# Kernel tuning notes

Hardware: AMD Instinct MI355X
Metric: run time of the kernel (lower is better)

Reference implementation:

```python
import jax, jax.numpy as jnp
import numpy as np

B, D, F, K = 16384, 768, 8192, 32

def setup_inputs() -> dict:
    key = jax.random.key(0)
    k0, k1, k2 = jax.random.split(key, 3)
    x = jax.random.normal(k0, (B, D), dtype=jnp.float32)
    # encoder weight ~ orthogonal-ish scale; exact init scheme doesn't affect the math being tested
    W_enc = jax.random.normal(k1, (F, D), dtype=jnp.float32) / np.sqrt(D)
    b_enc = jnp.zeros((F,), dtype=jnp.float32)
    W_dec = jax.random.normal(k2, (D, F), dtype=jnp.float32)
    # torch init normalizes decoder.weight rows (dim=1)
    W_dec = W_dec / jnp.linalg.norm(W_dec, axis=1, keepdims=True)
    dec_bias = jnp.zeros((D,), dtype=jnp.float32)
    return {"x": x, "W_enc": W_enc, "b_enc": b_enc, "W_dec": W_dec, "dec_bias": dec_bias, "k": K}


def reference(x, W_enc, b_enc, W_dec, dec_bias, k):
    # encode: center, linear, relu
    x_centered = x - dec_bias                              # [B, D]
    acts = jax.nn.relu(jnp.einsum('bd,fd->bf', x_centered, W_enc) + b_enc)  # [B, F]
    # topk + scatter into dense sparse code
    vals, idx = jax.lax.top_k(acts, k)                     # [B, k]
    rows = jnp.arange(acts.shape[0])[:, None]              # [B, 1]
    sparse_code = jnp.zeros_like(acts).at[rows, idx].set(vals)  # [B, F]
    # decode: dense GEMM over mostly-zero code + bias
    reconstruction = jnp.einsum('bf,df->bd', sparse_code, W_dec) + dec_bias  # [B, D]
    return reconstruction, sparse_code
```

## Files before the change

### kernel.cpp

```cpp
#include <hip/hip_runtime.h>

#define NB 16384
#define ND 768
#define NF 8192
#define CMAX 512
#define SEGW 16
#define GSEG 1024
#define AMAX 128
#define MARG 0.07f
#define THETA0 2.0f
#define THETA0_BITS 0x4000u

typedef __attribute__((ext_vector_type(8))) short bf16x8;
typedef __attribute__((ext_vector_type(4))) float f32x4;
typedef __attribute__((ext_vector_type(4))) unsigned int u32x4;
typedef __attribute__((ext_vector_type(2))) float f32x2;

__device__ inline unsigned short f2bf(float f) {
  unsigned u = __float_as_uint(f);
  unsigned r = (u + 0x7FFFu + ((u >> 16) & 1u)) >> 16;
  return (unsigned short)r;
}
__device__ inline float bfbits2f(unsigned u16) { return __uint_as_float(u16 << 16); }

__global__ __launch_bounds__(256) void cvt_bf16_k(const float* __restrict__ in,
                                                  unsigned short* __restrict__ out) {
  size_t t = (size_t)blockIdx.x * 256 + threadIdx.x;
  const float4* i4 = (const float4*)in;
  float4 a = i4[t * 2], b = i4[t * 2 + 1];
  ushort4 lo = make_ushort4(f2bf(a.x), f2bf(a.y), f2bf(a.z), f2bf(a.w));
  ushort4 hi = make_ushort4(f2bf(b.x), f2bf(b.y), f2bf(b.z), f2bf(b.w));
  ((ushort4*)out)[t * 2] = lo;
  ((ushort4*)out)[t * 2 + 1] = hi;
}

__global__ __launch_bounds__(256) void beta_k(const float* __restrict__ W_enc,
                                              const float* __restrict__ b_enc,
                                              const float* __restrict__ dec_bias,
                                              float* __restrict__ beta) {
  int f = blockIdx.x * 4 + (threadIdx.x >> 6);
  int lane = threadIdx.x & 63;
  const float* wr = W_enc + (size_t)f * ND;
  float s = 0.f;
  for (int d = lane; d < ND; d += 64) s += dec_bias[d] * wr[d];
  for (int off = 32; off; off >>= 1) s += __shfl_down(s, off);
  if (lane == 0) beta[f] = b_enc[f] - s;
}

__global__ __launch_bounds__(256) void transpose_bf_k(const float* __restrict__ in,
                                                      unsigned short* __restrict__ out) {
  __shared__ float tile[32][33];
  int lx = threadIdx.x & 31;
  int ty = threadIdx.x >> 5;
  int x = blockIdx.x * 32 + lx;
  for (int j = ty; j < 32; j += 8) {
    int y = blockIdx.y * 32 + j;
    tile[j][lx] = in[(size_t)y * NF + x];
  }
  __syncthreads();
  int xo = blockIdx.y * 32 + lx;
  for (int j = ty; j < 32; j += 8) {
    int yo = blockIdx.x * 32 + j;
    out[(size_t)yo * ND + xo] = f2bf(tile[lx][j]);
  }
}

__global__ __launch_bounds__(256) void enc_gemm_bf16(
    const unsigned short* __restrict__ Xb, const unsigned short* __restrict__ Wb,
    const float* __restrict__ beta, unsigned* __restrict__ glist) {
  __shared__ __align__(1024) unsigned short As[2][128 * 64];
  __shared__ __align__(1024) unsigned short Bs[2][128 * 64];
  __shared__ unsigned wseg[128][SEGW];
  __shared__ unsigned wcnt[128];
  const int tid = threadIdx.x;
  const int wave = tid >> 6, lane = tid & 63;
  const int wm = wave >> 1, wn = wave & 1;

  const int orig = blockIdx.y * gridDim.x + blockIdx.x;
  const int xcd = orig & 7;
  const int local = orig >> 3;
  const int tcol = local >> 4;
  const int trow = (xcd << 4) + (local & 15);
  const int brow = trow << 7;
  const int bcol = tcol << 7;

  f32x4 acc[4][4] = {};

  const int srow = tid >> 3;
  const int scol = (((tid & 7) ^ ((tid >> 3) & 7)) << 3);
  const unsigned short* gA = Xb + (size_t)(brow + srow) * ND + scol;
  const unsigned short* gB = Wb + (size_t)(bcol + srow) * ND + scol;

#pragma unroll
  for (int i = 0; i < 8; ++i) ((unsigned*)wseg)[tid + 256 * i] = 0u;
  if (tid < 128) wcnt[tid] = 0u;

#define STAGE(bufsel, kt)                                                      \
  _Pragma("unroll")                                                            \
  for (int i = 0; i < 4; ++i) {                                                \
    __builtin_amdgcn_global_load_lds(                                          \
        (const __attribute__((address_space(1))) void*)(gA + (size_t)(i * 32) * ND + (kt)), \
        (__attribute__((address_space(3))) void*)(As[bufsel] + (i * 32 + wave * 8) * 64), 16, 0, 0); \
    __builtin_amdgcn_global_load_lds(                                          \
        (const __attribute__((address_space(1))) void*)(gB + (size_t)(i * 32) * ND + (kt)), \
        (__attribute__((address_space(3))) void*)(Bs[bufsel] + (i * 32 + wave * 8) * 64), 16, 0, 0); \
  }

  STAGE(0, 0)
  __syncthreads();
  int cur = 0;
#pragma unroll 1
  for (int step = 0; step < 12; ++step) {
    if (step < 11) { STAGE(cur ^ 1, (step + 1) * 64) }
#pragma unroll
    for (int kk = 0; kk < 64; kk += 32) {
      const int chunk = (kk + ((lane >> 4) << 3)) >> 3;
      const int rA = (wm << 6) + (lane & 15);
      const int rB = (wn << 6) + (lane & 15);
      const int sw = chunk ^ (lane & 7);
      bf16x8 a[4], bvv[4];
#pragma unroll
      for (int m = 0; m < 4; ++m)
        a[m] = *(const bf16x8*)&As[cur][(rA + (m << 4)) * 64 + (sw << 3)];
#pragma unroll
      for (int n = 0; n < 4; ++n)
        bvv[n] = *(const bf16x8*)&Bs[cur][(rB + (n << 4)) * 64 + (sw << 3)];
#pragma unroll
      for (int m = 0; m < 4; ++m)
#pragma unroll
        for (int n = 0; n < 4; ++n)
          acc[m][n] = __builtin_amdgcn_mfma_f32_16x16x32_bf16(a[m], bvv[n], acc[m][n], 0, 0, 0);
    }
    if (step < 11) {
      __syncthreads();
      cur ^= 1;
    }
  }

#pragma unroll
  for (int n = 0; n < 4; ++n) {
    float bet = beta[bcol + (wn << 6) + (n << 4) + (lane & 15)];
#pragma unroll
    for (int m = 0; m < 4; ++m) {
#pragma unroll
      for (int r = 0; r < 4; ++r) {
        int row_l = (wm << 6) + (m << 4) + ((lane >> 4) << 2) + r;
        int col_l = (wn << 6) + (n << 4) + (lane & 15);
        float v = fmaxf(acc[m][n][r] + bet, 0.f);
        unsigned short ub = f2bf(v);
        if (ub >= (unsigned short)THETA0_BITS) {
          unsigned p = atomicAdd(&wcnt[row_l], 1u);
          if (p < SEGW) wseg[row_l][p] = ((unsigned)ub << 16) | (unsigned)(bcol + col_l);
        }
      }
    }
  }
  __syncthreads();
  {
    int row = tid >> 1;
    int sbase = (tid & 1) << 3;
    u32x4 v0 = *(const u32x4*)&wseg[row][sbase];
    u32x4 v1 = *(const u32x4*)&wseg[row][sbase + 4];
    if (sbase == 0 && wcnt[row] > SEGW) v0[0] = 0xFFFFFFFFu;
    unsigned* dst = &glist[(size_t)(brow + row) * GSEG + (tcol << 4)];
    __builtin_nontemporal_store(v0, (u32x4*)&dst[sbase]);
    __builtin_nontemporal_store(v1, (u32x4*)&dst[sbase + 4]);
  }
}

__global__ __launch_bounds__(256, 6) void ksel_k(
    const unsigned* __restrict__ glist,
    const float* __restrict__ x, const float* __restrict__ W_enc,
    const float* __restrict__ beta, const unsigned short* __restrict__ WdecBf,
    const float* __restrict__ dec_bias, const int* __restrict__ kptr,
    float* __restrict__ out_rec, float* __restrict__ g_vals, int* __restrict__ g_idxs) {
  const int tid = threadIdx.x, wave = tid >> 6, lane = tid & 63;
  const int b = blockIdx.x * 4 + wave;
  int k = *kptr; k = k < 1 ? 1 : (k > 64 ? 64 : k);
  const unsigned kk = (unsigned)k;

  __shared__ unsigned clist_s[4][CMAX];
  __shared__ unsigned long long aval_s[4][AMAX];
  __shared__ float selv_s[4][64];
  __shared__ int seli_s[4][64];
  __shared__ int ctrC_s[4], ctrW_s[4], ctrA_s[4];
  __shared__ int blkFb;
  __shared__ float fb_x[ND];
  __shared__ unsigned long long fbl[512];
  __shared__ unsigned fb_thrmax[256];
  __shared__ unsigned long long fb_red[4];
  __shared__ unsigned fb_cnt4[4];
  __shared__ unsigned fbcnt;

  unsigned* clist = clist_s[wave];
  unsigned long long* aval = aval_s[wave];
  float* selv = selv_s[wave];
  int* seli = seli_s[wave];

  if (tid == 0) blkFb = 0;
  if (lane == 0) { ctrC_s[wave] = 0; ctrW_s[wave] = 0; ctrA_s[wave] = 0; }

  bool bad = false;
  {
    const u32x4* seg4 = (const u32x4*)(glist + (size_t)b * GSEG);
#pragma unroll
    for (int ii = 0; ii < 4; ++ii) {
      u32x4 e4 = __builtin_nontemporal_load(&seg4[lane + (ii << 6)]);
#pragma unroll
      for (int q = 0; q < 4; ++q) {
        unsigned e = e4[q];
        if (e) {
          if ((e & 0xFFFFu) >= (unsigned)NF) bad = true;
          else {
            int p = atomicAdd(&ctrC_s[wave], 1);
            if (p < CMAX) clist[p] = e;
          }
        }
      }
    }
  }
  bad = (__ballot(bad) != 0ull);
  int n = ctrC_s[wave]; if (n > CMAX) n = CMAX;

  unsigned ks[8];
#pragma unroll
  for (int ii = 0; ii < 8; ++ii) {
    int j = lane + (ii << 6);
    ks[ii] = (j < n) ? (clist[j] >> 16) : 0u;
  }
  unsigned T = 0;
  for (int bit = 14; bit >= 0; --bit) {
    unsigned probe = T | (1u << bit);
    int c = 0;
#pragma unroll
    for (int ii = 0; ii < 8; ++ii) c += (ks[ii] >= probe);
#pragma unroll
    for (int off = 32; off; off >>= 1) c += __shfl_xor(c, off);
    if (c >= (int)kk) T = probe;
  }
  float tauf = bfbits2f(T);

  bool valid = !bad && (n >= k) && (tauf >= THETA0 + MARG);
  if (lane == 0 && !valid) atomicOr(&blkFb, 1);
  __syncthreads();

  if (!blkFb) {
    const float thrW = tauf + MARG;
    const float thrA = tauf - MARG;
    for (int j = lane; j < n; j += 64) {
      unsigned e = clist[j];
      float v = bfbits2f(e >> 16);
      int idx = (int)(e & 0xFFFFu);
      if (v > thrW) {
        int p = atomicAdd(&ctrW_s[wave], 1);
        if (p < 63) { selv[p] = v; seli[p] = idx; }
      } else if (v >= thrA) {
        int p = atomicAdd(&ctrA_s[wave], 1);
        if (p < AMAX) aval[p] = (unsigned long long)(unsigned)idx;
      }
    }
    __syncthreads();
    int c = ctrW_s[wave]; if (c > 63) c = 63; if (c > k - 1) c = k - 1;
    int na = ctrA_s[wave]; if (na > AMAX) na = AMAX;

    float xr[12];
#pragma unroll
    for (int cc = 0; cc < 12; ++cc)
      xr[cc] = __builtin_nontemporal_load(&x[(size_t)b * ND + lane + 64 * cc]);
    for (int j = 0; j < na; j += 2) {
      int f0 = (int)(unsigned)aval[j];
      int f1 = (j + 1 < na) ? (int)(unsigned)aval[j + 1] : f0;
      const float* w0 = W_enc + (size_t)f0 * ND;
      const float* w1 = W_enc + (size_t)f1 * ND;
      float s0 = 0.f, s1 = 0.f;
#pragma unroll
      for (int cc = 0; cc < 12; ++cc) {
        s0 = fmaf(xr[cc], w0[lane + 64 * cc], s0);
        s1 = fmaf(xr[cc], w1[lane + 64 * cc], s1);
      }
#pragma unroll
      for (int off = 32; off; off >>= 1) {
        s0 += __shfl_xor(s0, off);
        s1 += __shfl_xor(s1, off);
      }
      if (lane == 0) {
        float v0 = fmaxf(s0 + beta[f0], 0.f);
        aval[j] = (((unsigned long long)__float_as_uint(v0)) << 13) | (unsigned)(8191 - f0);
        if (j + 1 < na) {
          float v1 = fmaxf(s1 + beta[f1], 0.f);
          aval[j + 1] = (((unsigned long long)__float_as_uint(v1)) << 13) | (unsigned)(8191 - f1);
        }
      }
    }
    __syncthreads();

    unsigned long long p0 = (lane < na) ? aval[lane] : 0ull;
    unsigned long long p1 = (lane + 64 < na) ? aval[lane + 64] : 0ull;
    int rounds = k - c; if (rounds < 0) rounds = 0;
    for (int r = 0; r < rounds; ++r) {
      unsigned long long m = p0 > p1 ? p0 : p1;
#pragma unroll
      for (int off = 32; off; off >>= 1) {
        unsigned long long o = __shfl_xor(m, off);
        if (o > m) m = o;
      }
      if (lane == 0) {
        if (m) { selv[c + r] = __uint_as_float((unsigned)(m >> 13)); seli[c + r] = 8191 - (int)(m & 0x1FFFull); }
        else   { selv[c + r] = 0.f; seli[c + r] = 0; }
      }
      if (p0 == m) p0 = 0;
      if (p1 == m) p1 = 0;
    }
    __syncthreads();
  } else {
    for (int r = 0; r < 4; ++r) {
      const int row = blockIdx.x * 4 + r;
      fb_x[tid] = x[(size_t)row * ND + tid];
      fb_x[tid + 256] = x[(size_t)row * ND + tid + 256];
      fb_x[tid + 512] = x[(size_t)row * ND + tid + 512];
      __syncthreads();
      unsigned mymax = 0u;
      for (int j = 0; j < 32; ++j) {
        int f = tid * 32 + j;
        const float* w = W_enc + (size_t)f * ND;
        float s = 0.f;
#pragma unroll 8
        for (int d = 0; d < ND; ++d) s = fmaf(fb_x[d], w[d], s);
        unsigned bits = __float_as_uint(fmaxf(s + beta[f], 0.f));
        if (bits > mymax) mymax = bits;
      }
      fb_thrmax[tid] = mymax;
      __syncthreads();
      unsigned L = 0;
      for (int bit = 30; bit >= 0; --bit) {
        unsigned probe = L | (1u << bit);
        unsigned long long bl = __ballot(fb_thrmax[tid] >= probe);
        if (lane == 0) fb_cnt4[wave] = (unsigned)__popcll(bl);
        __syncthreads();
        unsigned tot = fb_cnt4[0] + fb_cnt4[1] + fb_cnt4[2] + fb_cnt4[3];
        if (tot >= kk) L = probe;
        __syncthreads();
      }
      if (tid == 0) fbcnt = 0u;
      __syncthreads();
      for (int j = 0; j < 32; ++j) {
        int f = tid * 32 + j;
        const float* w = W_enc + (size_t)f * ND;
        float s = 0.f;
#pragma unroll 8
        for (int d = 0; d < ND; ++d) s = fmaf(fb_x[d], w[d], s);
        unsigned bits = __float_as_uint(fmaxf(s + beta[f], 0.f));
        if (bits >= L) {
          unsigned p = atomicAdd(&fbcnt, 1u);
          if (p < 512) fbl[p] = (((unsigned long long)bits) << 13) | (unsigned)(8191 - f);
        }
      }
      __syncthreads();
      int n2 = (int)(fbcnt < 512u ? fbcnt : 512u);
      for (int rr = 0; rr < k; ++rr) {
        unsigned long long best = 0ull;
        for (int j2 = tid; j2 < n2; j2 += 256)
          if (fbl[j2] > best) best = fbl[j2];
#pragma unroll
        for (int off = 32; off; off >>= 1) {
          unsigned long long o = __shfl_xor(best, off);
          if (o > best) best = o;
        }
        if (lane == 0) fb_red[wave] = best;
        __syncthreads();
        unsigned long long m = fb_red[0];
#pragma unroll
        for (int w2 = 1; w2 < 4; ++w2)
          if (fb_red[w2] > m) m = fb_red[w2];
        if (tid == 0) {
          if (m) { selv_s[r][rr] = __uint_as_float((unsigned)(m >> 13)); seli_s[r][rr] = 8191 - (int)(m & 0x1FFFull); }
          else   { selv_s[r][rr] = 0.f; seli_s[r][rr] = 0; }
        }
        for (int j2 = tid; j2 < n2; j2 += 256)
          if (fbl[j2] == m) fbl[j2] = 0ull;
        __syncthreads();
      }
      __syncthreads();
    }
  }

  if (lane < k) {
    g_vals[(size_t)b * 64 + lane] = selv[lane];
    g_idxs[(size_t)b * 64 + lane] = seli[lane];
  }

  float acc[12];
#pragma unroll
  for (int cc = 0; cc < 6; ++cc) {
    float2 db = *(const float2*)&dec_bias[cc * 128 + lane * 2];
    acc[2 * cc] = db.x; acc[2 * cc + 1] = db.y;
  }
#define RECON_TERM(r)                                                          \
  {                                                                            \
    int f = seli[r]; float v = selv[r];                                        \
    const unsigned short* wd = WdecBf + (size_t)f * ND;                        \
    _Pragma("unroll")                                                          \
    for (int cc = 0; cc < 6; ++cc) {                                           \
      unsigned pr = *(const unsigned*)&wd[cc * 128 + lane * 2];                \
      acc[2 * cc] = fmaf(v, bfbits2f(pr & 0xFFFFu), acc[2 * cc]);              \
      acc[2 * cc + 1] = fmaf(v, bfbits2f(pr >> 16), acc[2 * cc + 1]);          \
    }                                                                          \
  }
  if (k == 32) {
#pragma unroll
    for (int r = 0; r < 32; ++r) RECON_TERM(r)
  } else {
    for (int r = 0; r < k; ++r) RECON_TERM(r)
  }
#pragma unroll
  for (int cc = 0; cc < 6; ++cc) {
    f32x2 st = {acc[2 * cc], acc[2 * cc + 1]};
    __builtin_nontemporal_store(st, (f32x2*)&out_rec[(size_t)b * ND + cc * 128 + lane * 2]);
  }
}

__global__ __launch_bounds__(256) void d2_sparse_k(
    const float* __restrict__ g_vals, const int* __restrict__ g_idxs,
    const int* __restrict__ kptr, float* __restrict__ out_sc) {
  const int b = blockIdx.x, tid = threadIdx.x;
  int k = *kptr; k = k < 1 ? 1 : (k > 64 ? 64 : k);
  __shared__ float row[NF];
  __shared__ float sv[64];
  __shared__ int si[64];
  if (tid < k) { sv[tid] = g_vals[(size_t)b * 64 + tid]; si[tid] = g_idxs[(size_t)b * 64 + tid]; }
  float4* r4 = (float4*)row;
#pragma unroll
  for (int i = 0; i < 8; ++i) r4[tid + 256 * i] = make_float4(0.f, 0.f, 0.f, 0.f);
  __syncthreads();
  if (tid < k) row[si[tid]] = sv[tid];
  __syncthreads();
  f32x4* o4 = (f32x4*)(out_sc + (size_t)b * NF);
  const f32x4* r4v = (const f32x4*)row;
#pragma unroll
  for (int i = 0; i < 8; ++i)
    __builtin_nontemporal_store(r4v[tid + 256 * i], &o4[tid + 256 * i]);
}

extern "C" void kernel_launch(void* const* d_in, const int* in_sizes, int n_in,
                              void* d_out, int out_size, void* d_ws, size_t ws_size,
                              hipStream_t stream) {
  const float* x        = (const float*)d_in[0];
  const float* W_enc    = (const float*)d_in[1];
  const float* b_enc    = (const float*)d_in[2];
  const float* W_dec    = (const float*)d_in[3];
  const float* dec_bias = (const float*)d_in[4];
  const int*   kptr     = (const int*)d_in[5];

  float* out_rec = (float*)d_out;
  float* out_sc  = (float*)d_out + (size_t)NB * ND;

  char* scb = (char*)out_sc;
  unsigned*       glist = (unsigned*)scb;
  unsigned short* Xbf   = (unsigned short*)(scb + 67108864);
  unsigned short* Wbf   = (unsigned short*)(scb + 92274688);

  char* ws = (char*)d_ws;
  unsigned short* WdecBf = (unsigned short*)ws;
  float* beta   = (float*)(ws + 12582912);
  float* g_vals = (float*)(ws + 12615680);
  int*   g_idxs = (int*)(ws + 16809984);

  cvt_bf16_k<<<(NB * ND) / 2048, 256, 0, stream>>>(x, Xbf);
  cvt_bf16_k<<<(NF * ND) / 2048, 256, 0, stream>>>(W_enc, Wbf);
  beta_k<<<NF / 4, 256, 0, stream>>>(W_enc, b_enc, dec_bias, beta);
  transpose_bf_k<<<dim3(NF / 32, ND / 32), 256, 0, stream>>>(W_dec, WdecBf);
  enc_gemm_bf16<<<dim3(NF / 128, NB / 128), 256, 0, stream>>>(Xbf, Wbf, beta, glist);
  ksel_k<<<NB / 4, 256, 0, stream>>>(glist, x, W_enc, beta, WdecBf, dec_bias, kptr,
                                     out_rec, g_vals, g_idxs);
  d2_sparse_k<<<NB, 256, 0, stream>>>(g_vals, g_idxs, kptr, out_sc);
}
```

Before: 646.9 us.

## Single-buffer encoder GEMM LDS and alias top-k staging into A tile

The encoder GEMM's double-buffered LDS tiles become single-buffered, with a barrier after each load and after each compute step. The per-row candidate segment and count arrays are moved into the A-tile shared memory once the K loop has finished. This roughly halves the kernel's LDS footprint, so more workgroups can be resident per CU and hide global-load latency that way. The cost is losing the explicit prefetch of the next K slice behind the current MFMAs, plus an extra barrier per iteration.

```diff
diff --git a/kernel.cpp b/kernel.cpp
--- a/kernel.cpp
+++ b/kernel.cpp
@@ -68,10 +68,8 @@
 __global__ __launch_bounds__(256) void enc_gemm_bf16(
     const unsigned short* __restrict__ Xb, const unsigned short* __restrict__ Wb,
     const float* __restrict__ beta, unsigned* __restrict__ glist) {
-  __shared__ __align__(1024) unsigned short As[2][128 * 64];
-  __shared__ __align__(1024) unsigned short Bs[2][128 * 64];
-  __shared__ unsigned wseg[128][SEGW];
-  __shared__ unsigned wcnt[128];
+  __shared__ __align__(1024) unsigned short As[128 * 64];
+  __shared__ __align__(1024) unsigned short Bs[128 * 64];
   const int tid = threadIdx.x;
   const int wave = tid >> 6, lane = tid & 63;
   const int wm = wave >> 1, wn = wave & 1;
@@ -91,27 +89,19 @@
   const unsigned short* gA = Xb + (size_t)(brow + srow) * ND + scol;
   const unsigned short* gB = Wb + (size_t)(bcol + srow) * ND + scol;
 
-#pragma unroll
-  for (int i = 0; i < 8; ++i) ((unsigned*)wseg)[tid + 256 * i] = 0u;
-  if (tid < 128) wcnt[tid] = 0u;
-
-#define STAGE(bufsel, kt)                                                      \
-  _Pragma("unroll")                                                            \
-  for (int i = 0; i < 4; ++i) {                                                \
-    __builtin_amdgcn_global_load_lds(                                          \
-        (const __attribute__((address_space(1))) void*)(gA + (size_t)(i * 32) * ND + (kt)), \
-        (__attribute__((address_space(3))) void*)(As[bufsel] + (i * 32 + wave * 8) * 64), 16, 0, 0); \
-    __builtin_amdgcn_global_load_lds(                                          \
-        (const __attribute__((address_space(1))) void*)(gB + (size_t)(i * 32) * ND + (kt)), \
-        (__attribute__((address_space(3))) void*)(Bs[bufsel] + (i * 32 + wave * 8) * 64), 16, 0, 0); \
-  }
-
-  STAGE(0, 0)
-  __syncthreads();
-  int cur = 0;
 #pragma unroll 1
   for (int step = 0; step < 12; ++step) {
-    if (step < 11) { STAGE(cur ^ 1, (step + 1) * 64) }
+    const int kt = step * 64;
+#pragma unroll
+    for (int i = 0; i < 4; ++i) {
+      __builtin_amdgcn_global_load_lds(
+          (const __attribute__((address_space(1))) void*)(gA + (size_t)(i * 32) * ND + kt),
+          (__attribute__((address_space(3))) void*)(As + (i * 32 + wave * 8) * 64), 16, 0, 0);
+      __builtin_amdgcn_global_load_lds(
+          (const __attribute__((address_space(1))) void*)(gB + (size_t)(i * 32) * ND + kt),
+          (__attribute__((address_space(3))) void*)(Bs + (i * 32 + wave * 8) * 64), 16, 0, 0);
+    }
+    __syncthreads();
 #pragma unroll
     for (int kk = 0; kk < 64; kk += 32) {
       const int chunk = (kk + ((lane >> 4) << 3)) >> 3;
@@ -121,21 +111,25 @@
       bf16x8 a[4], bvv[4];
 #pragma unroll
       for (int m = 0; m < 4; ++m)
-        a[m] = *(const bf16x8*)&As[cur][(rA + (m << 4)) * 64 + (sw << 3)];
+        a[m] = *(const bf16x8*)&As[(rA + (m << 4)) * 64 + (sw << 3)];
 #pragma unroll
       for (int n = 0; n < 4; ++n)
-        bvv[n] = *(const bf16x8*)&Bs[cur][(rB + (n << 4)) * 64 + (sw << 3)];
+        bvv[n] = *(const bf16x8*)&Bs[(rB + (n << 4)) * 64 + (sw << 3)];
 #pragma unroll
       for (int m = 0; m < 4; ++m)
 #pragma unroll
         for (int n = 0; n < 4; ++n)
           acc[m][n] = __builtin_amdgcn_mfma_f32_16x16x32_bf16(a[m], bvv[n], acc[m][n], 0, 0, 0);
     }
-    if (step < 11) {
-      __syncthreads();
-      cur ^= 1;
-    }
-  }
+    __syncthreads();
+  }
+
+  unsigned (*wseg)[SEGW] = (unsigned (*)[SEGW])As;
+  unsigned* wcnt = (unsigned*)(As + 4096);
+#pragma unroll
+  for (int i = 0; i < 8; ++i) ((unsigned*)wseg)[tid + 256 * i] = 0u;
+  if (tid < 128) wcnt[tid] = 0u;
+  __syncthreads();
 
 #pragma unroll
   for (int n = 0; n < 4; ++n) {
```

Result: faster. 571.8 us (-11.6%).
